# Kernel optimization log

Hardware: AMD Instinct MI355X
Metric: run time of the kernel (lower is better)

Reference implementation:

```python
import jax, jax.numpy as jnp
import numpy as np

N_NODES = 100000
N_EDGES = 1600000
IN_C, HID, OUT_C = 128, 128, 64
LN_EPS = 1e-5


def _glorot(key, shape):
    fan_in = shape[-1]
    return jax.random.normal(key, shape, dtype=jnp.float32) / jnp.sqrt(jnp.float32(fan_in))


def setup_inputs() -> dict:
    key = jax.random.key(0)
    ks = jax.random.split(key, 16)
    x = jax.random.normal(ks[0], (N_NODES, IN_C), dtype=jnp.float32)
    edge_index = jax.random.randint(ks[1], (2, N_EDGES), 0, N_NODES, dtype=jnp.int64)
    inp = {"x": x, "edge_index": edge_index}
    dims = [(IN_C, HID), (HID, HID), (HID, OUT_C)]
    for i, (din, dout) in enumerate(dims):
        inp[f"Wl{i}"] = _glorot(ks[2 + 3 * i], (dout, din))   # neighbor-aggregate weight
        inp[f"Wr{i}"] = _glorot(ks[3 + 3 * i], (dout, din))   # root/self weight
        inp[f"b{i}"] = jnp.zeros((dout,), dtype=jnp.float32)
    for i, d in enumerate([HID, HID]):
        inp[f"g{i}"] = jnp.ones((d,), dtype=jnp.float32)      # LayerNorm gamma
        inp[f"be{i}"] = jnp.zeros((d,), dtype=jnp.float32)    # LayerNorm beta
    return inp


def sage_conv(x, src, dst, Wl, Wr, b):
    # mean aggregation of source features at destination nodes
    msg = x[src]                                                    # [E, F]
    agg = jax.ops.segment_sum(msg, dst, num_segments=N_NODES)      # [N, F]
    deg = jax.ops.segment_sum(jnp.ones((src.shape[0],), x.dtype), dst, num_segments=N_NODES)
    agg = agg / jnp.maximum(deg, 1.0)[:, None]
    return agg @ Wl.T + x @ Wr.T + b


def layer_norm(x, gamma, beta):
    mu = jnp.mean(x, axis=-1, keepdims=True)
    var = jnp.mean(jnp.square(x - mu), axis=-1, keepdims=True)
    return (x - mu) * jax.lax.rsqrt(var + LN_EPS) * gamma + beta


def reference(x, edge_index, Wl0, Wr0, b0, g0, be0, Wl1, Wr1, b1, g1, be1, Wl2, Wr2, b2):
    src, dst = edge_index[0], edge_index[1]
    h = layer_norm(jax.nn.relu(sage_conv(x, src, dst, Wl0, Wr0, b0)), g0, be0)
    h = layer_norm(jax.nn.relu(sage_conv(h, src, dst, Wl1, Wr1, b1)), g1, be1)
    return sage_conv(h, src, dst, Wl2, Wr2, b2)
```

## Files before the change

kernel.cpp:

```cpp
#include <hip/hip_runtime.h>


typedef __bf16    bf16x8 __attribute__((ext_vector_type(8)));
typedef __bf16    bf16x4 __attribute__((ext_vector_type(4)));
typedef float     f32x4  __attribute__((ext_vector_type(4)));
typedef _Float16  f16x2  __attribute__((ext_vector_type(2)));

#define PB_SHIFT 9
#define PB_NB    256
#define PB_EPT   8
#define PB_BLOCK 256
#define PB_CHUNK (PB_BLOCK * PB_EPT)

__global__ __launch_bounds__(PB_BLOCK) void coarse_hist(
    const int* __restrict__ dst, int* __restrict__ bhist, int E) {
    __shared__ int h[PB_NB];
    const int t = threadIdx.x;
    h[t] = 0;
    __syncthreads();
    const int e0 = blockIdx.x * PB_CHUNK + t;
#pragma unroll
    for (int i = 0; i < PB_EPT; ++i) {
        int e = e0 + i * PB_BLOCK;
        if (e < E) atomicAdd(&h[dst[e] >> PB_SHIFT], 1);
    }
    __syncthreads();
    if (h[t]) atomicAdd(&bhist[t], h[t]);
}

__global__ __launch_bounds__(PB_NB) void coarse_scan(
    const int* __restrict__ bhist, int* __restrict__ bbase, int* __restrict__ bcur) {
    __shared__ int sm[PB_NB];
    const int t = threadIdx.x;
    int v = bhist[t];
    sm[t] = v;
    __syncthreads();
    for (int off = 1; off < PB_NB; off <<= 1) {
        int add = (t >= off) ? sm[t - off] : 0;
        __syncthreads();
        sm[t] += add;
        __syncthreads();
    }
    int excl = sm[t] - v;
    bbase[t] = excl;
    bcur[t] = excl;
}

__global__ __launch_bounds__(PB_BLOCK) void part_scatter(
    const int* __restrict__ src, const int* __restrict__ dst,
    int* __restrict__ bcursor, int2* __restrict__ part, int E) {
    __shared__ int hist[PB_NB];
    __shared__ int base[PB_NB];
    const int t = threadIdx.x;
    hist[t] = 0;
    __syncthreads();
    const int e0 = blockIdx.x * PB_CHUNK + t;
    int my_s[PB_EPT], my_d[PB_EPT], my_r[PB_EPT];
#pragma unroll
    for (int i = 0; i < PB_EPT; ++i) {
        int e = e0 + i * PB_BLOCK;
        if (e < E) {
            my_s[i] = src[e];
            my_d[i] = dst[e];
            my_r[i] = atomicAdd(&hist[my_d[i] >> PB_SHIFT], 1);
        }
    }
    __syncthreads();
    {
        int c = hist[t];
        base[t] = c ? atomicAdd(&bcursor[t], c) : 0;
    }
    __syncthreads();
#pragma unroll
    for (int i = 0; i < PB_EPT; ++i) {
        int e = e0 + i * PB_BLOCK;
        if (e < E) {
            int b = my_d[i] >> PB_SHIFT;
            part[base[b] + my_r[i]] = make_int2(my_s[i], my_d[i]);
        }
    }
}

__global__ __launch_bounds__(256) void bucket_build(
    const int2* __restrict__ part, const int* __restrict__ bbase,
    int* __restrict__ offs, int* __restrict__ ssrc, int N, int E) {
    __shared__ int h[512];
    __shared__ int s[512];
    __shared__ int cur[512];
    const int b = blockIdx.x;
    const int t = threadIdx.x;
    const int beg = bbase[b];
    const int end = (b == PB_NB - 1) ? E : bbase[b + 1];

    h[t] = 0; h[t + 256] = 0;
    __syncthreads();
    for (int e = beg + t; e < end; e += 256)
        atomicAdd(&h[part[e].y & 511], 1);
    __syncthreads();
    s[t] = h[t]; s[t + 256] = h[t + 256];
    __syncthreads();
    for (int off = 1; off < 512; off <<= 1) {
        int a0 = (t >= off) ? s[t - off] : 0;
        int i1 = t + 256;
        int a1 = (i1 >= off) ? s[i1 - off] : 0;
        __syncthreads();
        s[t] += a0; s[i1] += a1;
        __syncthreads();
    }
#pragma unroll
    for (int k = 0; k < 2; ++k) {
        int i = t + k * 256;
        int excl = s[i] - h[i];
        cur[i] = excl;
        int node = (b << PB_SHIFT) + i;
        if (node < N) offs[node] = beg + excl;
    }
    if (b == 0 && t == 0) offs[N] = E;
    __syncthreads();
    for (int e = beg + t; e < end; e += 256) {
        int2 sd = part[e];
        int p = atomicAdd(&cur[sd.y & 511], 1);
        ssrc[beg + p] = sd.x;
    }
}

template <int DOUT, typename AT, typename ZT>
__global__ __launch_bounds__(256) void gemm_mfma(
    const AT* __restrict__ A,
    const float* __restrict__ Wl,
    const float* __restrict__ Wr,
    const float* __restrict__ bias,
    _Float16* __restrict__ ybuf,
    ZT*       __restrict__ zbuf,
    int M) {
    __shared__ __bf16 Asm[64 * 136];
    __shared__ __bf16 Bsm[DOUT * 136];

    const int t = threadIdx.x;
    const int rowBase = blockIdx.x * 64;

    if constexpr (sizeof(AT) == 4) {
#pragma unroll
        for (int i = 0; i < 8; ++i) {
            int idx = t + 256 * i;
            int r = idx >> 5;
            int c4 = idx & 31;
            int grow = rowBase + r;
            if (grow >= M) grow = M - 1;
            float4 v = *(const float4*)((const float*)A + (size_t)grow * 128 + c4 * 4);
            bf16x4 o;
            o[0] = (__bf16)v.x; o[1] = (__bf16)v.y; o[2] = (__bf16)v.z; o[3] = (__bf16)v.w;
            *(bf16x4*)(Asm + r * 136 + c4 * 4) = o;
        }
    } else {
#pragma unroll
        for (int i = 0; i < 4; ++i) {
            int idx = t + 256 * i;
            int r = idx >> 4;
            int c8 = idx & 15;
            int grow = rowBase + r;
            if (grow >= M) grow = M - 1;
            bf16x8 v = *(const bf16x8*)((const __bf16*)A + (size_t)grow * 128 + c8 * 8);
            *(bf16x8*)(Asm + r * 136 + c8 * 8) = v;
        }
    }

    const int lane = t & 63;
    const int wid = t >> 6;
    const int mb = (wid >> 1) * 32;
    const int nbase = (wid & 1) * (DOUT / 2);
    constexpr int NJ = DOUT / 32;
    const int ln = lane & 15;
    const int qk = lane >> 4;
    constexpr int BCH = DOUT * 32 / 256;

#pragma unroll
    for (int phase = 0; phase < 2; ++phase) {
        const bool isZ = phase != 0;
        const float* W = isZ ? Wr : Wl;

#pragma unroll
        for (int i = 0; i < BCH; ++i) {
            int idx = t + 256 * i;
            int r = idx >> 5;
            int c4 = idx & 31;
            float4 v = *(const float4*)(W + (size_t)r * 128 + c4 * 4);
            bf16x4 o;
            o[0] = (__bf16)v.x; o[1] = (__bf16)v.y; o[2] = (__bf16)v.z; o[3] = (__bf16)v.w;
            *(bf16x4*)(Bsm + r * 136 + c4 * 4) = o;
        }
        __syncthreads();

        f32x4 acc[2][NJ] = {};
#pragma unroll
        for (int ks = 0; ks < 4; ++ks) {
            const int k0 = ks * 32 + qk * 8;
            bf16x8 a0 = *(const bf16x8*)(Asm + (mb + ln) * 136 + k0);
            bf16x8 a1 = *(const bf16x8*)(Asm + (mb + 16 + ln) * 136 + k0);
            bf16x8 b[NJ];
#pragma unroll
            for (int j = 0; j < NJ; ++j)
                b[j] = *(const bf16x8*)(Bsm + (nbase + j * 16 + ln) * 136 + k0);
#pragma unroll
            for (int j = 0; j < NJ; ++j) {
                acc[0][j] = __builtin_amdgcn_mfma_f32_16x16x32_bf16(a0, b[j], acc[0][j], 0, 0, 0);
                acc[1][j] = __builtin_amdgcn_mfma_f32_16x16x32_bf16(a1, b[j], acc[1][j], 0, 0, 0);
            }
        }

        float bcol[NJ];
        if (isZ) {
#pragma unroll
            for (int j = 0; j < NJ; ++j) bcol[j] = bias[nbase + j * 16 + ln];
        }
#pragma unroll
        for (int i = 0; i < 2; ++i) {
#pragma unroll
            for (int r = 0; r < 4; ++r) {
                int grow = rowBase + mb + i * 16 + qk * 4 + r;
                if (grow >= M) continue;
#pragma unroll
                for (int j = 0; j < NJ; ++j) {
                    int col = nbase + j * 16 + ln;
                    float v = acc[i][j][r];
                    if (isZ) zbuf[(size_t)grow * DOUT + col] = (ZT)(v + bcol[j]);
                    else     ybuf[(size_t)grow * DOUT + col] = (_Float16)v;
                }
            }
        }
        __syncthreads();
    }
}

__global__ __launch_bounds__(256) void agg_ln128(
    const int* __restrict__ offs, const int* __restrict__ ssrc,
    const _Float16* __restrict__ ybuf,
    const __bf16* __restrict__ zbuf,
    const float* __restrict__ gamma, const float* __restrict__ beta,
    __bf16* __restrict__ hout, int nNodes) {
    const int lane = threadIdx.x & 63;
    const int qh = lane >> 4;
    const int li = lane & 15;
    const int node = blockIdx.x * 4 + (threadIdx.x >> 6);
    if (node >= nNodes) return;
    const int beg = offs[node], end = offs[node + 1];
    const int deg = end - beg;

    f16x2 pacc[4] = {};
    const int iters = (deg + 7) >> 3;
    int eA = beg + qh;
    int eB = eA + 4;
    int idxA = 0, idxB = 0;
    if (iters > 0) {
        idxA = ssrc[(eA < end) ? eA : beg];
        idxB = ssrc[(eB < end) ? eB : beg];
    }
    for (int u = 0; u < iters; ++u) {
        const bool va = eA < end;
        const bool vb = eB < end;
        uint4 wa, wb;
        if (va) wa = *(const uint4*)(ybuf + (size_t)idxA * 128 + li * 8);
        if (vb) wb = *(const uint4*)(ybuf + (size_t)idxB * 128 + li * 8);
        int eA2 = eA + 8, eB2 = eB + 8;
        int idxA2 = ssrc[(eA2 < end) ? eA2 : beg];
        int idxB2 = ssrc[(eB2 < end) ? eB2 : beg];
        if (va) {
            pacc[0] += *(const f16x2*)&wa.x;
            pacc[1] += *(const f16x2*)&wa.y;
            pacc[2] += *(const f16x2*)&wa.z;
            pacc[3] += *(const f16x2*)&wa.w;
        }
        if (vb) {
            pacc[0] += *(const f16x2*)&wb.x;
            pacc[1] += *(const f16x2*)&wb.y;
            pacc[2] += *(const f16x2*)&wb.z;
            pacc[3] += *(const f16x2*)&wb.w;
        }
        eA = eA2; eB = eB2; idxA = idxA2; idxB = idxB2;
    }

    bf16x8 zv = *(const bf16x8*)(zbuf + (size_t)node * 128 + li * 8);
    const float4* g4 = (const float4*)(gamma + li * 8);
    const float4* b4 = (const float4*)(beta + li * 8);
    float4 g0 = g4[0], g1 = g4[1], bb0 = b4[0], bb1 = b4[1];

#pragma unroll
    for (int m = 0; m < 4; ++m) {
        int w = *(const int*)&pacc[m];
        int w1 = __shfl_xor(w, 16, 64);
        pacc[m] += *(const f16x2*)&w1;
        w = *(const int*)&pacc[m];
        int w2 = __shfl_xor(w, 32, 64);
        pacc[m] += *(const f16x2*)&w2;
    }
    float acc[8];
#pragma unroll
    for (int m = 0; m < 4; ++m) {
        acc[2 * m]     = (float)pacc[m][0];
        acc[2 * m + 1] = (float)pacc[m][1];
    }
    float inv = 1.f / (float)((deg > 1) ? deg : 1);
    float v[8];
#pragma unroll
    for (int m = 0; m < 8; ++m) v[m] = fmaxf(acc[m] * inv + (float)zv[m], 0.f);

    float s = 0.f;
#pragma unroll
    for (int m = 0; m < 8; ++m) s += v[m];
#pragma unroll
    for (int off = 8; off >= 1; off >>= 1) s += __shfl_xor(s, off, 64);
    float mu = s * (1.f / 128.f);
    float d[8], q = 0.f;
#pragma unroll
    for (int m = 0; m < 8; ++m) { d[m] = v[m] - mu; q += d[m] * d[m]; }
#pragma unroll
    for (int off = 8; off >= 1; off >>= 1) q += __shfl_xor(q, off, 64);
    float rstd = rsqrtf(q * (1.f / 128.f) + 1e-5f);

    if (qh == 0) {
        bf16x8 o;
        o[0] = (__bf16)(d[0] * rstd * g0.x + bb0.x);
        o[1] = (__bf16)(d[1] * rstd * g0.y + bb0.y);
        o[2] = (__bf16)(d[2] * rstd * g0.z + bb0.z);
        o[3] = (__bf16)(d[3] * rstd * g0.w + bb0.w);
        o[4] = (__bf16)(d[4] * rstd * g1.x + bb1.x);
        o[5] = (__bf16)(d[5] * rstd * g1.y + bb1.y);
        o[6] = (__bf16)(d[6] * rstd * g1.z + bb1.z);
        o[7] = (__bf16)(d[7] * rstd * g1.w + bb1.w);
        *(bf16x8*)(hout + (size_t)node * 128 + li * 8) = o;
    }
}

__global__ __launch_bounds__(256) void agg_out64(
    const int* __restrict__ offs, const int* __restrict__ ssrc,
    const _Float16* __restrict__ ybuf,
    const float* __restrict__ zbuf,
    float* __restrict__ out, int nNodes) {
    const int lane = threadIdx.x & 63;
    const int qh = lane >> 4;
    const int li = lane & 15;
    const int node = blockIdx.x * 4 + (threadIdx.x >> 6);
    if (node >= nNodes) return;
    const int beg = offs[node], end = offs[node + 1];
    const int deg = end - beg;

    f16x2 pacc[2] = {};
    const int iters = (deg + 7) >> 3;
    int eA = beg + qh;
    int eB = eA + 4;
    int idxA = 0, idxB = 0;
    if (iters > 0) {
        idxA = ssrc[(eA < end) ? eA : beg];
        idxB = ssrc[(eB < end) ? eB : beg];
    }
    for (int u = 0; u < iters; ++u) {
        const bool va = eA < end;
        const bool vb = eB < end;
        uint2 wa, wb;
        if (va) wa = *(const uint2*)(ybuf + (size_t)idxA * 64 + li * 4);
        if (vb) wb = *(const uint2*)(ybuf + (size_t)idxB * 64 + li * 4);
        int eA2 = eA + 8, eB2 = eB + 8;
        int idxA2 = ssrc[(eA2 < end) ? eA2 : beg];
        int idxB2 = ssrc[(eB2 < end) ? eB2 : beg];
        if (va) {
            pacc[0] += *(const f16x2*)&wa.x;
            pacc[1] += *(const f16x2*)&wa.y;
        }
        if (vb) {
            pacc[0] += *(const f16x2*)&wb.x;
            pacc[1] += *(const f16x2*)&wb.y;
        }
        eA = eA2; eB = eB2; idxA = idxA2; idxB = idxB2;
    }

    const float4* z4 = (const float4*)(zbuf + (size_t)node * 64 + li * 4);
    float4 z0 = z4[0];

#pragma unroll
    for (int m = 0; m < 2; ++m) {
        int w = *(const int*)&pacc[m];
        int w1 = __shfl_xor(w, 16, 64);
        pacc[m] += *(const f16x2*)&w1;
        w = *(const int*)&pacc[m];
        int w2 = __shfl_xor(w, 32, 64);
        pacc[m] += *(const f16x2*)&w2;
    }
    if (qh == 0) {
        float inv = 1.f / (float)((deg > 1) ? deg : 1);
        float4 o;
        o.x = (float)pacc[0][0] * inv + z0.x;
        o.y = (float)pacc[0][1] * inv + z0.y;
        o.z = (float)pacc[1][0] * inv + z0.z;
        o.w = (float)pacc[1][1] * inv + z0.w;
        *(float4*)(out + (size_t)node * 64 + li * 4) = o;
    }
}

extern "C" void kernel_launch(void* const* d_in, const int* in_sizes, int n_in,
                              void* d_out, int out_size, void* d_ws, size_t ws_size,
                              hipStream_t stream) {
    const float* x   = (const float*)d_in[0];
    const int*   ei  = (const int*)d_in[1];
    const float* Wl0 = (const float*)d_in[2];
    const float* Wr0 = (const float*)d_in[3];
    const float* b0  = (const float*)d_in[4];
    const float* Wl1 = (const float*)d_in[5];
    const float* Wr1 = (const float*)d_in[6];
    const float* b1  = (const float*)d_in[7];
    const float* Wl2 = (const float*)d_in[8];
    const float* Wr2 = (const float*)d_in[9];
    const float* b2  = (const float*)d_in[10];
    const float* g0  = (const float*)d_in[11];
    const float* be0 = (const float*)d_in[12];
    const float* g1  = (const float*)d_in[13];
    const float* be1 = (const float*)d_in[14];

    const int N = in_sizes[0] / 128;
    const int E = in_sizes[1] / 2;
    const int* src = ei;
    const int* dst = ei + E;
    float* out = (float*)d_out;

    char* p = (char*)d_ws;
    auto carve = [&](size_t bytes) {
        void* q = (void*)p;
        p += (bytes + 255) & ~(size_t)255;
        return q;
    };
    int*      offs  = (int*)carve(sizeof(int) * (size_t)(N + 1));
    int*      bhist = (int*)carve(sizeof(int) * (size_t)PB_NB);
    int*      bbase = (int*)carve(sizeof(int) * (size_t)PB_NB);
    int*      bcur  = (int*)carve(sizeof(int) * (size_t)PB_NB);
    int*      ssrc  = (int*)carve(sizeof(int) * (size_t)E);
    int2*     part  = (int2*)carve(sizeof(int2) * (size_t)E);
    __bf16*   h     = (__bf16*)carve(sizeof(__bf16) * (size_t)N * 128);
    _Float16* ybuf  = (_Float16*)carve(sizeof(_Float16) * (size_t)N * 128);
    void*     zraw  = carve(sizeof(__bf16) * (size_t)N * 128);
    __bf16*   zb    = (__bf16*)zraw;
    float*    zf    = (float*)zraw;

    (void)hipMemsetAsync(bhist, 0, sizeof(int) * PB_NB, stream);
    const int gridE = (E + PB_CHUNK - 1) / PB_CHUNK;
    coarse_hist<<<gridE, PB_BLOCK, 0, stream>>>(dst, bhist, E);
    coarse_scan<<<1, PB_NB, 0, stream>>>(bhist, bbase, bcur);
    part_scatter<<<gridE, PB_BLOCK, 0, stream>>>(src, dst, bcur, part, E);
    bucket_build<<<PB_NB, 256, 0, stream>>>(part, bbase, offs, ssrc, N, E);

    const int gridM = (N + 63) / 64;
    const int gridNode = (N + 3) / 4;

    gemm_mfma<128, float, __bf16><<<gridM, 256, 0, stream>>>(x, Wl0, Wr0, b0, ybuf, zb, N);
    agg_ln128<<<gridNode, 256, 0, stream>>>(offs, ssrc, ybuf, zb, g0, be0, h, N);
    gemm_mfma<128, __bf16, __bf16><<<gridM, 256, 0, stream>>>(h, Wl1, Wr1, b1, ybuf, zb, N);
    agg_ln128<<<gridNode, 256, 0, stream>>>(offs, ssrc, ybuf, zb, g1, be1, h, N);
    gemm_mfma<64, __bf16, float><<<gridM, 256, 0, stream>>>(h, Wl2, Wr2, b2, ybuf, zf, N);
    agg_out64<<<gridNode, 256, 0, stream>>>(offs, ssrc, ybuf, zf, out, N);
}
```

Baseline: 427.9 us.

## Make GEMM persistent with resident weights and double-buffered A tiles

```diff
diff --git a/kernel.cpp b/kernel.cpp
--- a/kernel.cpp
+++ b/kernel.cpp
@@ -125,7 +125,7 @@
 }
 
 template <int DOUT, typename AT, typename ZT>
-__global__ __launch_bounds__(256) void gemm_mfma(
+__global__ __launch_bounds__(512) void gemm_mfma(
     const AT* __restrict__ A,
     const float* __restrict__ Wl,
     const float* __restrict__ Wr,
@@ -133,37 +133,56 @@
     _Float16* __restrict__ ybuf,
     ZT*       __restrict__ zbuf,
     int M) {
-    __shared__ __bf16 Asm[64 * 136];
-    __shared__ __bf16 Bsm[DOUT * 136];
+    __shared__ __bf16 Asm[2][128 * 136];
+    __shared__ __bf16 Wsm[2][DOUT * 136];
 
     const int t = threadIdx.x;
-    const int rowBase = blockIdx.x * 64;
-
-    if constexpr (sizeof(AT) == 4) {
-#pragma unroll
-        for (int i = 0; i < 8; ++i) {
-            int idx = t + 256 * i;
+    const int nt = (M + 127) >> 7;
+
+    constexpr int WCH = DOUT * 32 / 512;
+#pragma unroll
+    for (int wsel = 0; wsel < 2; ++wsel) {
+        const float* W = wsel ? Wr : Wl;
+#pragma unroll
+        for (int i = 0; i < WCH; ++i) {
+            int idx = t + 512 * i;
             int r = idx >> 5;
             int c4 = idx & 31;
-            int grow = rowBase + r;
-            if (grow >= M) grow = M - 1;
-            float4 v = *(const float4*)((const float*)A + (size_t)grow * 128 + c4 * 4);
+            float4 v = *(const float4*)(W + (size_t)r * 128 + c4 * 4);
             bf16x4 o;
             o[0] = (__bf16)v.x; o[1] = (__bf16)v.y; o[2] = (__bf16)v.z; o[3] = (__bf16)v.w;
-            *(bf16x4*)(Asm + r * 136 + c4 * 4) = o;
-        }
-    } else {
-#pragma unroll
-        for (int i = 0; i < 4; ++i) {
-            int idx = t + 256 * i;
-            int r = idx >> 4;
-            int c8 = idx & 15;
-            int grow = rowBase + r;
-            if (grow >= M) grow = M - 1;
-            bf16x8 v = *(const bf16x8*)((const __bf16*)A + (size_t)grow * 128 + c8 * 8);
-            *(bf16x8*)(Asm + r * 136 + c8 * 8) = v;
-        }
-    }
+            *(bf16x4*)(Wsm[wsel] + r * 136 + c4 * 4) = o;
+        }
+    }
+
+    auto stageA = [&](int buf, int tile) {
+        const int rowBase = tile << 7;
+        if constexpr (sizeof(AT) == 4) {
+#pragma unroll
+            for (int i = 0; i < 8; ++i) {
+                int idx = t + 512 * i;
+                int r = idx >> 5;
+                int c4 = idx & 31;
+                int grow = rowBase + r;
+                if (grow >= M) grow = M - 1;
+                float4 v = *(const float4*)((const float*)A + (size_t)grow * 128 + c4 * 4);
+                bf16x4 o;
+                o[0] = (__bf16)v.x; o[1] = (__bf16)v.y; o[2] = (__bf16)v.z; o[3] = (__bf16)v.w;
+                *(bf16x4*)(Asm[buf] + r * 136 + c4 * 4) = o;
+            }
+        } else {
+#pragma unroll
+            for (int i = 0; i < 4; ++i) {
+                int idx = t + 512 * i;
+                int r = idx >> 4;
+                int c8 = idx & 15;
+                int grow = rowBase + r;
+                if (grow >= M) grow = M - 1;
+                bf16x8 v = *(const bf16x8*)((const __bf16*)A + (size_t)grow * 128 + c8 * 8);
+                *(bf16x8*)(Asm[buf] + r * 136 + c8 * 8) = v;
+            }
+        }
+    };
 
     const int lane = t & 63;
     const int wid = t >> 6;
@@ -172,63 +191,58 @@
     constexpr int NJ = DOUT / 32;
     const int ln = lane & 15;
     const int qk = lane >> 4;
-    constexpr int BCH = DOUT * 32 / 256;
-
-#pragma unroll
-    for (int phase = 0; phase < 2; ++phase) {
-        const bool isZ = phase != 0;
-        const float* W = isZ ? Wr : Wl;
-
-#pragma unroll
-        for (int i = 0; i < BCH; ++i) {
-            int idx = t + 256 * i;
-            int r = idx >> 5;
-            int c4 = idx & 31;
-            float4 v = *(const float4*)(W + (size_t)r * 128 + c4 * 4);
-            bf16x4 o;
-            o[0] = (__bf16)v.x; o[1] = (__bf16)v.y; o[2] = (__bf16)v.z; o[3] = (__bf16)v.w;
-            *(bf16x4*)(Bsm + r * 136 + c4 * 4) = o;
-        }
-        __syncthreads();
-
-        f32x4 acc[2][NJ] = {};
-#pragma unroll
-        for (int ks = 0; ks < 4; ++ks) {
-            const int k0 = ks * 32 + qk * 8;
-            bf16x8 a0 = *(const bf16x8*)(Asm + (mb + ln) * 136 + k0);
-            bf16x8 a1 = *(const bf16x8*)(Asm + (mb + 16 + ln) * 136 + k0);
-            bf16x8 b[NJ];
-#pragma unroll
-            for (int j = 0; j < NJ; ++j)
-                b[j] = *(const bf16x8*)(Bsm + (nbase + j * 16 + ln) * 136 + k0);
-#pragma unroll
-            for (int j = 0; j < NJ; ++j) {
-                acc[0][j] = __builtin_amdgcn_mfma_f32_16x16x32_bf16(a0, b[j], acc[0][j], 0, 0, 0);
-                acc[1][j] = __builtin_amdgcn_mfma_f32_16x16x32_bf16(a1, b[j], acc[1][j], 0, 0, 0);
-            }
-        }
-
-        float bcol[NJ];
-        if (isZ) {
-#pragma unroll
-            for (int j = 0; j < NJ; ++j) bcol[j] = bias[nbase + j * 16 + ln];
-        }
-#pragma unroll
-        for (int i = 0; i < 2; ++i) {
-#pragma unroll
-            for (int r = 0; r < 4; ++r) {
-                int grow = rowBase + mb + i * 16 + qk * 4 + r;
-                if (grow >= M) continue;
+
+    float bcol[NJ];
+#pragma unroll
+    for (int j = 0; j < NJ; ++j) bcol[j] = bias[nbase + j * 16 + ln];
+
+    int tile = blockIdx.x;
+    if (tile >= nt) return;
+    int buf = 0;
+    stageA(0, tile);
+    __syncthreads();
+
+    for (; tile < nt; tile += gridDim.x) {
+        const int next = tile + gridDim.x;
+        if (next < nt) stageA(buf ^ 1, next);
+
+        const int rowBase = tile << 7;
+#pragma unroll
+        for (int ph = 0; ph < 2; ++ph) {
+            f32x4 acc[2][NJ] = {};
+#pragma unroll
+            for (int ks = 0; ks < 4; ++ks) {
+                const int k0 = ks * 32 + qk * 8;
+                bf16x8 a0 = *(const bf16x8*)(Asm[buf] + (mb + ln) * 136 + k0);
+                bf16x8 a1 = *(const bf16x8*)(Asm[buf] + (mb + 16 + ln) * 136 + k0);
+                bf16x8 b[NJ];
+#pragma unroll
+                for (int j = 0; j < NJ; ++j)
+                    b[j] = *(const bf16x8*)(Wsm[ph] + (nbase + j * 16 + ln) * 136 + k0);
 #pragma unroll
                 for (int j = 0; j < NJ; ++j) {
-                    int col = nbase + j * 16 + ln;
-                    float v = acc[i][j][r];
-                    if (isZ) zbuf[(size_t)grow * DOUT + col] = (ZT)(v + bcol[j]);
-                    else     ybuf[(size_t)grow * DOUT + col] = (_Float16)v;
+                    acc[0][j] = __builtin_amdgcn_mfma_f32_16x16x32_bf16(a0, b[j], acc[0][j], 0, 0, 0);
+                    acc[1][j] = __builtin_amdgcn_mfma_f32_16x16x32_bf16(a1, b[j], acc[1][j], 0, 0, 0);
                 }
             }
+#pragma unroll
+            for (int i = 0; i < 2; ++i) {
+#pragma unroll
+                for (int r = 0; r < 4; ++r) {
+                    int grow = rowBase + mb + i * 16 + qk * 4 + r;
+                    if (grow >= M) continue;
+#pragma unroll
+                    for (int j = 0; j < NJ; ++j) {
+                        int col = nbase + j * 16 + ln;
+                        float v = acc[i][j][r];
+                        if (ph) zbuf[(size_t)grow * DOUT + col] = (ZT)(v + bcol[j]);
+                        else    ybuf[(size_t)grow * DOUT + col] = (_Float16)v;
+                    }
+                }
+            }
         }
         __syncthreads();
+        buf ^= 1;
     }
 }
 
@@ -446,13 +460,13 @@
     part_scatter<<<gridE, PB_BLOCK, 0, stream>>>(src, dst, bcur, part, E);
     bucket_build<<<PB_NB, 256, 0, stream>>>(part, bbase, offs, ssrc, N, E);
 
-    const int gridM = (N + 63) / 64;
     const int gridNode = (N + 3) / 4;
-
-    gemm_mfma<128, float, __bf16><<<gridM, 256, 0, stream>>>(x, Wl0, Wr0, b0, ybuf, zb, N);
+    const int gridG = 256;
+
+    gemm_mfma<128, float, __bf16><<<gridG, 512, 0, stream>>>(x, Wl0, Wr0, b0, ybuf, zb, N);
     agg_ln128<<<gridNode, 256, 0, stream>>>(offs, ssrc, ybuf, zb, g0, be0, h, N);
-    gemm_mfma<128, __bf16, __bf16><<<gridM, 256, 0, stream>>>(h, Wl1, Wr1, b1, ybuf, zb, N);
+    gemm_mfma<128, __bf16, __bf16><<<gridG, 512, 0, stream>>>(h, Wl1, Wr1, b1, ybuf, zb, N);
     agg_ln128<<<gridNode, 256, 0, stream>>>(offs, ssrc, ybuf, zb, g1, be1, h, N);
-    gemm_mfma<64, __bf16, float><<<gridM, 256, 0, stream>>>(h, Wl2, Wr2, b2, ybuf, zf, N);
+    gemm_mfma<64, __bf16, float><<<gridG, 512, 0, stream>>>(h, Wl2, Wr2, b2, ybuf, zf, N);
     agg_out64<<<gridNode, 256, 0, stream>>>(offs, ssrc, ybuf, zf, out, N);
 }
```

After: 423.6 us. About the same (-1.0%).
